# Kernel tuning notes

Hardware: AMD Instinct MI355X
Metric: run time of the kernel (lower is better)

Reference implementation:

```python
import jax, jax.numpy as jnp
import numpy as np

N_OPS = 32
D_REASON = 128
TOP_K = 2
EPS = 1e-05
LEAK = 1e-05  # coefficient on the all-ops leak term


def setup_inputs() -> dict:
    key = jax.random.key(0)
    k1, k2, k3, k4 = jax.random.split(key, 4)
    B, S = 8, 2048
    x = jax.random.normal(k1, (B, S, D_REASON), dtype=jnp.float32)
    indices = jax.random.randint(k2, (B, S, TOP_K), 0, N_OPS, dtype=jnp.int64)
    weights = jax.random.uniform(k3, (B, S, TOP_K), dtype=jnp.float32)
    ops = 0.02 * jax.random.normal(k4, (N_OPS, D_REASON, D_REASON), dtype=jnp.float32)
    return {"x": x, "indices": indices, "weights": weights, "ops": ops}


def _ternary_effective(ops):
    # scale_n = clamp(mean|W_n|, 1e-5); q = STE ternary quantize; W_eff = q * scale
    scale = jnp.maximum(jnp.mean(jnp.abs(ops), axis=(1, 2)), EPS)  # (N,)
    q_hard = jnp.clip(jnp.round(ops / scale[:, None, None]), -1.0, 1.0)
    # STE: identity gradient w.r.t. ops through the quantizer
    q = ops + jax.lax.stop_gradient(q_hard - ops)
    return q * scale[:, None, None]  # (N, D, D)


def reference(x, indices, weights, ops):
    # x: (B,S,D); indices: (B,S,K) int; weights: (B,S,K); ops: (N,D,D)
    w_eff = _ternary_effective(ops)  # (N, D_out, D_in)
    # F.linear(x, W) = x @ W.T, for every op at once -> T: (B,S,N,D_out)
    T = jnp.einsum("bsd,nod->bsno", x, w_eff)
    total = T.sum(axis=2)  # sum over all ops, (B,S,D)
    # gather the selected top_k ops per token: (B,S,K,D)
    gathered = jnp.take_along_axis(T, indices[..., None].astype(jnp.int32), axis=2)
    routed = jnp.sum(weights[..., None] * gathered, axis=2)  # (B,S,D)
    return LEAK * total / N_OPS + routed
```

## Files before the change

### kernel.cpp

```cpp
#include <hip/hip_runtime.h>

#define N_OPS 32
#define D 128
#define MAT (D * D)
#define EPS 1e-5f
#define LEAK 1e-5f
#define NTOK (8 * 2048)
#define NASSIGN (NTOK * 2)
#define CAP 34816
#define EXP_GRPS (CAP / 64)
#define LEAK_BLKS 64

typedef __attribute__((ext_vector_type(8))) short short8;
typedef __attribute__((ext_vector_type(4))) float f32x4;

__device__ inline unsigned short f2bf(float f) {
    unsigned int u = __float_as_uint(f);
    return (unsigned short)((u + 0x7FFF + ((u >> 16) & 1)) >> 16);
}
__device__ inline float bf2f(unsigned short h) {
    return __uint_as_float(((unsigned int)h) << 16);
}

__global__ __launch_bounds__(256) void k_prep(const float* __restrict__ ops,
                                              const int* __restrict__ idx,
                                              const float* __restrict__ x,
                                              float* __restrict__ scale,
                                              int* __restrict__ hist2,
                                              unsigned short* __restrict__ xb) {
    if (blockIdx.x < N_OPS) {
        const int n = blockIdx.x;
        const float* W = ops + n * MAT;
        float s = 0.f;
        for (int i = threadIdx.x; i < MAT; i += 256) s += fabsf(W[i]);
        for (int off = 32; off; off >>= 1) s += __shfl_xor(s, off);
        __shared__ float red[4];
        const int lane = threadIdx.x & 63, wid = threadIdx.x >> 6;
        if (lane == 0) red[wid] = s;
        __syncthreads();
        if (threadIdx.x == 0)
            scale[n] = fmaxf((red[0] + red[1] + red[2] + red[3]) / (float)MAT, EPS);
    } else if (blockIdx.x < 64) {
        const int b = blockIdx.x - N_OPS;
        __shared__ int lh[N_OPS];
        if (threadIdx.x < N_OPS) lh[threadIdx.x] = 0;
        __syncthreads();
#pragma unroll
        for (int j = 0; j < 4; ++j)
            atomicAdd(&lh[idx[b * 1024 + j * 256 + threadIdx.x]], 1);
        __syncthreads();
        if (threadIdx.x < N_OPS) hist2[b * N_OPS + threadIdx.x] = lh[threadIdx.x];
    } else {
        const int gid = (blockIdx.x - 64) * 256 + threadIdx.x;
        const float4* xp = (const float4*)(x + (size_t)gid * 8);
        float4 a = xp[0], b = xp[1];
        unsigned short o[8] = {f2bf(a.x), f2bf(a.y), f2bf(a.z), f2bf(a.w),
                               f2bf(b.x), f2bf(b.y), f2bf(b.z), f2bf(b.w)};
        ((short8*)xb)[gid] = *(const short8*)o;
    }
}

__global__ __launch_bounds__(256) void k_scan_quant(const float* __restrict__ ops,
                                                    const float* __restrict__ scale,
                                                    const int* __restrict__ hist2,
                                                    int* __restrict__ base2,
                                                    int* __restrict__ list,
                                                    unsigned short* __restrict__ wb) {
    if (blockIdx.x == 0) {
        __shared__ int hl[1024];
        __shared__ int totl[N_OPS];
        __shared__ int offl[N_OPS + 1];
        for (int i = threadIdx.x; i < 1024; i += 256) hl[i] = hist2[i];
        __syncthreads();
        if (threadIdx.x < N_OPS) {
            int t = 0;
            for (int b = 0; b < 32; ++b) t += hl[b * N_OPS + threadIdx.x];
            totl[threadIdx.x] = t;
        }
        __syncthreads();
        if (threadIdx.x == 0) {
            int run = 0;
            for (int e = 0; e < N_OPS; ++e) { offl[e] = run; run += (totl[e] + 63) & ~63; }
            offl[N_OPS] = run;
        }
        __syncthreads();
        if (threadIdx.x < N_OPS) {
            const int e = threadIdx.x;
            int running = offl[e];
            for (int b = 0; b < 32; ++b) { base2[b * N_OPS + e] = running; running += hl[b * N_OPS + e]; }
            for (int s = running; s < offl[e + 1]; ++s) list[s] = -1;
        }
        for (int s = offl[N_OPS] + (int)threadIdx.x; s < CAP; s += 256) list[s] = -1;
    } else {
        const int e = blockIdx.x - 1;
        const float sc = scale[e];
        const float* W = ops + e * MAT;
#pragma unroll
        for (int it = 0; it < 8; ++it) {
            const int f = it * 256 + threadIdx.x;
            const int o = f >> 4, dc = f & 15;
            const float4* wp = (const float4*)(W + o * D + dc * 8);
            float4 a = wp[0], b = wp[1];
            float v[8] = {a.x, a.y, a.z, a.w, b.x, b.y, b.z, b.w};
            unsigned short q[8];
#pragma unroll
            for (int j = 0; j < 8; ++j) {
                float t = rintf(v[j] / sc);
                t = fminf(1.f, fmaxf(-1.f, t));
                q[j] = (t == 0.f) ? 0 : (t > 0.f ? 0x3F80 : 0xBF80);
            }
            ((short8*)wb)[e * 2048 + dc * 128 + o] = *(const short8*)q;
        }
    }
}

__global__ __launch_bounds__(256) void k_scatter_leakmat(const int* __restrict__ idx,
                                                         const float* __restrict__ scale,
                                                         const int* __restrict__ base2,
                                                         int* __restrict__ list,
                                                         int* __restrict__ slot_of,
                                                         unsigned short* __restrict__ wb) {
    if (blockIdx.x < 32) {
        const int b = blockIdx.x;
        __shared__ int lh[N_OPS];
        if (threadIdx.x < N_OPS) lh[threadIdx.x] = 0;
        __syncthreads();
#pragma unroll
        for (int j = 0; j < 4; ++j) {
            const int a = b * 1024 + j * 256 + threadIdx.x;
            const int e = idx[a];
            const int r = atomicAdd(&lh[e], 1);
            const int slot = base2[b * N_OPS + e] + r;
            list[slot] = (e << 20) | a;
            slot_of[a] = slot;
        }
    } else {
        const int lb = blockIdx.x - 32;
        const int g  = lb * 32 + (threadIdx.x >> 3);
        const int ec = threadIdx.x & 7;
        float acc[8] = {0, 0, 0, 0, 0, 0, 0, 0};
#pragma unroll
        for (int ee = 0; ee < 4; ++ee) {
            const int e = ec * 4 + ee;
            const float se = scale[e];
            short8 v = ((const short8*)wb)[e * 2048 + g];
#pragma unroll
            for (int j = 0; j < 8; ++j) acc[j] += se * bf2f((unsigned short)v[j]);
        }
#pragma unroll
        for (int m = 1; m <= 4; m <<= 1)
#pragma unroll
            for (int j = 0; j < 8; ++j) acc[j] += __shfl_xor(acc[j], m);
        if (ec == 0) {
            unsigned short o[8];
#pragma unroll
            for (int j = 0; j < 8; ++j) o[j] = f2bf(acc[j] * (LEAK / (float)N_OPS));
            ((short8*)wb)[N_OPS * 2048 + g] = *(const short8*)o;
        }
    }
}

__global__ __launch_bounds__(256, 2) void k_mfma(const unsigned short* __restrict__ xb,
                                                 const int* __restrict__ list,
                                                 const unsigned short* __restrict__ wb,
                                                 const float* __restrict__ scale,
                                                 float* __restrict__ partial,
                                                 float* __restrict__ out) {
    __shared__ short8 lB[2048];
    const int lane = threadIdx.x & 63;
    const int wv   = threadIdx.x >> 6;
    const int quad = lane >> 4;
    const int ncol = lane & 15;

    const bool isleak = blockIdx.x >= EXP_GRPS;
    const short8* src;
    if (isleak) {
        src = (const short8*)wb + N_OPS * 2048;
    } else {
        const int v0 = list[blockIdx.x * 64];
        if (v0 < 0) return;
        src = (const short8*)wb + (v0 >> 20) * 2048;
    }
    for (int i = threadIdx.x; i < 2048; i += 256) lB[i] = src[i];
    __syncthreads();

    const int npass = isleak ? 4 : 1;
    for (int g = 0; g < npass; ++g) {
        int rowbase, tok;
        float sc;
        float* dst;
        if (isleak) {
            rowbase = (blockIdx.x - EXP_GRPS) * 256 + g * 64 + wv * 16;
            tok = rowbase + ncol;
            sc = 1.f;
            dst = out;
        } else {
            rowbase = blockIdx.x * 64 + wv * 16;
            const int v = list[rowbase + ncol];
            tok = (v < 0) ? 0 : ((v & 0xFFFFF) >> 1);
            sc = scale[__builtin_amdgcn_readfirstlane(list[blockIdx.x * 64]) >> 20];
            dst = partial;
        }
        const short8* Ap = (const short8*)(xb + (size_t)tok * D);

        f32x4 acc[8];
#pragma unroll
        for (int j = 0; j < 8; ++j) acc[j] = (f32x4){0.f, 0.f, 0.f, 0.f};

#pragma unroll
        for (int s = 0; s < 4; ++s) {
            const short8 a = Ap[s * 4 + quad];
            const short8* Bp = lB + (s * 4 + quad) * 128;
#pragma unroll
            for (int nt = 0; nt < 8; ++nt) {
                const short8 b = Bp[nt * 16 + ncol];
                acc[nt] = __builtin_amdgcn_mfma_f32_16x16x32_bf16(a, b, acc[nt], 0, 0, 0);
            }
        }
#pragma unroll
        for (int nt = 0; nt < 8; ++nt)
#pragma unroll
            for (int r = 0; r < 4; ++r)
                dst[(size_t)(rowbase + quad * 4 + r) * D + nt * 16 + ncol] = acc[nt][r] * sc;
    }
}

__global__ __launch_bounds__(256) void k_final(const float* __restrict__ partial,
                                               const int* __restrict__ slot_of,
                                               const float* __restrict__ wts,
                                               float* __restrict__ out) {
    const int lane = threadIdx.x & 63;
    const int t = blockIdx.x * 4 + (threadIdx.x >> 6);
    const int s0 = slot_of[2 * t], s1 = slot_of[2 * t + 1];
    const float w0 = wts[2 * t], w1 = wts[2 * t + 1];
    const float2 p0 = ((const float2*)(partial + (size_t)s0 * D))[lane];
    const float2 p1 = ((const float2*)(partial + (size_t)s1 * D))[lane];
    float2* op = ((float2*)out) + (size_t)t * 64 + lane;
    float2 o = *op;
    o.x += w0 * p0.x + w1 * p1.x;
    o.y += w0 * p0.y + w1 * p1.y;
    *op = o;
}

extern "C" void kernel_launch(void* const* d_in, const int* in_sizes, int n_in,
                              void* d_out, int out_size, void* d_ws, size_t ws_size,
                              hipStream_t stream) {
    const float* x   = (const float*)d_in[0];
    const int*   idx = (const int*)  d_in[1];
    const float* wts = (const float*)d_in[2];
    const float* ops = (const float*)d_in[3];
    float* out = (float*)d_out;

    float*          partial = (float*)d_ws;
    unsigned short* xb      = (unsigned short*)(partial + (size_t)CAP * D);
    unsigned short* wb      = xb + (size_t)NTOK * D;
    float*          scale   = (float*)(wb + 33 * MAT);
    int*            hist2   = (int*)(scale + 32);
    int*            base2   = hist2 + 1024;
    int*            list    = base2 + 1024;
    int*            slot_of = list + CAP;

    k_prep<<<1088, 256, 0, stream>>>(ops, idx, x, scale, hist2, xb);
    k_scan_quant<<<33, 256, 0, stream>>>(ops, scale, hist2, base2, list, wb);
    k_scatter_leakmat<<<96, 256, 0, stream>>>(idx, scale, base2, list, slot_of, wb);
    k_mfma<<<EXP_GRPS + LEAK_BLKS, 256, 0, stream>>>(xb, list, wb, scale, partial, out);
    k_final<<<NTOK / 4, 256, 0, stream>>>(partial, slot_of, wts, out);
}
```

Before: 110.3 us.

## Store expert and leak partials in bf16, fuse quantization into prep, enlarge expert blocks

Ternary quantization of the ops now runs inside the scale-reduction blocks of the prep kernel, and the leak matrix is built in the scan kernel. Expert groups are padded to 256 rows, so each MFMA block covers four 64-row passes with one shared B-tile load. Expert partials and leak results are written as bf16 to a separate buffer, and the final kernel combines them without a read-modify-write of out. This is meant to cut global memory traffic and stage count, at the cost of extra bf16 rounding on the partials and more padding rows.

```diff
diff --git a/kernel.cpp b/kernel.cpp
--- a/kernel.cpp
+++ b/kernel.cpp
@@ -7,8 +7,8 @@
 #define LEAK 1e-5f
 #define NTOK (8 * 2048)
 #define NASSIGN (NTOK * 2)
-#define CAP 34816
-#define EXP_GRPS (CAP / 64)
+#define CAP 40960
+#define EXP_BLKS (CAP / 256)
 #define LEAK_BLKS 64
 
 typedef __attribute__((ext_vector_type(8))) short short8;
@@ -27,19 +27,41 @@
                                               const float* __restrict__ x,
                                               float* __restrict__ scale,
                                               int* __restrict__ hist2,
-                                              unsigned short* __restrict__ xb) {
+                                              unsigned short* __restrict__ xb,
+                                              unsigned short* __restrict__ wb) {
     if (blockIdx.x < N_OPS) {
-        const int n = blockIdx.x;
-        const float* W = ops + n * MAT;
+        const int e = blockIdx.x;
+        const float* W = ops + e * MAT;
         float s = 0.f;
         for (int i = threadIdx.x; i < MAT; i += 256) s += fabsf(W[i]);
         for (int off = 32; off; off >>= 1) s += __shfl_xor(s, off);
         __shared__ float red[4];
+        __shared__ float s_scale;
         const int lane = threadIdx.x & 63, wid = threadIdx.x >> 6;
         if (lane == 0) red[wid] = s;
         __syncthreads();
-        if (threadIdx.x == 0)
-            scale[n] = fmaxf((red[0] + red[1] + red[2] + red[3]) / (float)MAT, EPS);
+        if (threadIdx.x == 0) {
+            s_scale = fmaxf((red[0] + red[1] + red[2] + red[3]) / (float)MAT, EPS);
+            scale[e] = s_scale;
+        }
+        __syncthreads();
+        const float sc = s_scale;
+#pragma unroll
+        for (int it = 0; it < 8; ++it) {
+            const int f = it * 256 + threadIdx.x;
+            const int o = f >> 4, dc = f & 15;
+            const float4* wp = (const float4*)(W + o * D + dc * 8);
+            float4 a = wp[0], b = wp[1];
+            float v[8] = {a.x, a.y, a.z, a.w, b.x, b.y, b.z, b.w};
+            unsigned short q[8];
+#pragma unroll
+            for (int j = 0; j < 8; ++j) {
+                float t = rintf(v[j] / sc);
+                t = fminf(1.f, fmaxf(-1.f, t));
+                q[j] = (t == 0.f) ? 0 : (t > 0.f ? 0x3F80 : 0xBF80);
+            }
+            ((short8*)wb)[e * 2048 + dc * 128 + o] = *(const short8*)q;
+        }
     } else if (blockIdx.x < 64) {
         const int b = blockIdx.x - N_OPS;
         __shared__ int lh[N_OPS];
@@ -60,12 +82,11 @@
     }
 }
 
-__global__ __launch_bounds__(256) void k_scan_quant(const float* __restrict__ ops,
-                                                    const float* __restrict__ scale,
-                                                    const int* __restrict__ hist2,
-                                                    int* __restrict__ base2,
-                                                    int* __restrict__ list,
-                                                    unsigned short* __restrict__ wb) {
+__global__ __launch_bounds__(256) void k_scan_leak(const int* __restrict__ hist2,
+                                                   const float* __restrict__ scale,
+                                                   int* __restrict__ base2,
+                                                   int* __restrict__ list,
+                                                   unsigned short* __restrict__ wb) {
     if (blockIdx.x == 0) {
         __shared__ int hl[1024];
         __shared__ int totl[N_OPS];
@@ -80,7 +101,7 @@
         __syncthreads();
         if (threadIdx.x == 0) {
             int run = 0;
-            for (int e = 0; e < N_OPS; ++e) { offl[e] = run; run += (totl[e] + 63) & ~63; }
+            for (int e = 0; e < N_OPS; ++e) { offl[e] = run; run += (totl[e] + 255) & ~255; }
             offl[N_OPS] = run;
         }
         __syncthreads();
@@ -90,52 +111,10 @@
             for (int b = 0; b < 32; ++b) { base2[b * N_OPS + e] = running; running += hl[b * N_OPS + e]; }
             for (int s = running; s < offl[e + 1]; ++s) list[s] = -1;
         }
+        __syncthreads();
         for (int s = offl[N_OPS] + (int)threadIdx.x; s < CAP; s += 256) list[s] = -1;
     } else {
-        const int e = blockIdx.x - 1;
-        const float sc = scale[e];
-        const float* W = ops + e * MAT;
-#pragma unroll
-        for (int it = 0; it < 8; ++it) {
-            const int f = it * 256 + threadIdx.x;
-            const int o = f >> 4, dc = f & 15;
-            const float4* wp = (const float4*)(W + o * D + dc * 8);
-            float4 a = wp[0], b = wp[1];
-            float v[8] = {a.x, a.y, a.z, a.w, b.x, b.y, b.z, b.w};
-            unsigned short q[8];
-#pragma unroll
-            for (int j = 0; j < 8; ++j) {
-                float t = rintf(v[j] / sc);
-                t = fminf(1.f, fmaxf(-1.f, t));
-                q[j] = (t == 0.f) ? 0 : (t > 0.f ? 0x3F80 : 0xBF80);
-            }
-            ((short8*)wb)[e * 2048 + dc * 128 + o] = *(const short8*)q;
-        }
-    }
-}
-
-__global__ __launch_bounds__(256) void k_scatter_leakmat(const int* __restrict__ idx,
-                                                         const float* __restrict__ scale,
-                                                         const int* __restrict__ base2,
-                                                         int* __restrict__ list,
-                                                         int* __restrict__ slot_of,
-                                                         unsigned short* __restrict__ wb) {
-    if (blockIdx.x < 32) {
-        const int b = blockIdx.x;
-        __shared__ int lh[N_OPS];
-        if (threadIdx.x < N_OPS) lh[threadIdx.x] = 0;
-        __syncthreads();
-#pragma unroll
-        for (int j = 0; j < 4; ++j) {
-            const int a = b * 1024 + j * 256 + threadIdx.x;
-            const int e = idx[a];
-            const int r = atomicAdd(&lh[e], 1);
-            const int slot = base2[b * N_OPS + e] + r;
-            list[slot] = (e << 20) | a;
-            slot_of[a] = slot;
-        }
-    } else {
-        const int lb = blockIdx.x - 32;
+        const int lb = blockIdx.x - 1;
         const int g  = lb * 32 + (threadIdx.x >> 3);
         const int ec = threadIdx.x & 7;
         float acc[8] = {0, 0, 0, 0, 0, 0, 0, 0};
@@ -160,46 +139,66 @@
     }
 }
 
+__global__ __launch_bounds__(256) void k_scatter(const int* __restrict__ idx,
+                                                 const int* __restrict__ base2,
+                                                 int* __restrict__ list,
+                                                 int* __restrict__ slot_of) {
+    const int b = blockIdx.x;
+    __shared__ int lh[N_OPS];
+    if (threadIdx.x < N_OPS) lh[threadIdx.x] = 0;
+    __syncthreads();
+#pragma unroll
+    for (int j = 0; j < 4; ++j) {
+        const int a = b * 1024 + j * 256 + threadIdx.x;
+        const int e = idx[a];
+        const int r = atomicAdd(&lh[e], 1);
+        const int slot = base2[b * N_OPS + e] + r;
+        list[slot] = (e << 20) | a;
+        slot_of[a] = slot;
+    }
+}
+
 __global__ __launch_bounds__(256, 2) void k_mfma(const unsigned short* __restrict__ xb,
                                                  const int* __restrict__ list,
                                                  const unsigned short* __restrict__ wb,
                                                  const float* __restrict__ scale,
-                                                 float* __restrict__ partial,
-                                                 float* __restrict__ out) {
+                                                 unsigned short* __restrict__ partial,
+                                                 unsigned short* __restrict__ lp) {
     __shared__ short8 lB[2048];
     const int lane = threadIdx.x & 63;
     const int wv   = threadIdx.x >> 6;
     const int quad = lane >> 4;
     const int ncol = lane & 15;
 
-    const bool isleak = blockIdx.x >= EXP_GRPS;
+    const bool isleak = blockIdx.x >= EXP_BLKS;
+    int base;
     const short8* src;
+    float sc;
+    unsigned short* dst;
     if (isleak) {
+        base = (blockIdx.x - EXP_BLKS) * 256;
         src = (const short8*)wb + N_OPS * 2048;
+        sc = 1.f;
+        dst = lp;
     } else {
-        const int v0 = list[blockIdx.x * 64];
+        base = blockIdx.x * 256;
+        const int v0 = list[base];
         if (v0 < 0) return;
         src = (const short8*)wb + (v0 >> 20) * 2048;
+        sc = scale[v0 >> 20];
+        dst = partial;
     }
     for (int i = threadIdx.x; i < 2048; i += 256) lB[i] = src[i];
     __syncthreads();
 
-    const int npass = isleak ? 4 : 1;
-    for (int g = 0; g < npass; ++g) {
-        int rowbase, tok;
-        float sc;
-        float* dst;
+    for (int g = 0; g < 4; ++g) {
+        const int rowbase = base + g * 64 + wv * 16;
+        int tok;
         if (isleak) {
-            rowbase = (blockIdx.x - EXP_GRPS) * 256 + g * 64 + wv * 16;
             tok = rowbase + ncol;
-            sc = 1.f;
-            dst = out;
         } else {
-            rowbase = blockIdx.x * 64 + wv * 16;
             const int v = list[rowbase + ncol];
             tok = (v < 0) ? 0 : ((v & 0xFFFFF) >> 1);
-            sc = scale[__builtin_amdgcn_readfirstlane(list[blockIdx.x * 64]) >> 20];
-            dst = partial;
         }
         const short8* Ap = (const short8*)(xb + (size_t)tok * D);
 
@@ -221,11 +220,13 @@
         for (int nt = 0; nt < 8; ++nt)
 #pragma unroll
             for (int r = 0; r < 4; ++r)
-                dst[(size_t)(rowbase + quad * 4 + r) * D + nt * 16 + ncol] = acc[nt][r] * sc;
-    }
-}
-
-__global__ __launch_bounds__(256) void k_final(const float* __restrict__ partial,
+                dst[(size_t)(rowbase + quad * 4 + r) * D + nt * 16 + ncol] =
+                    f2bf(acc[nt][r] * sc);
+    }
+}
+
+__global__ __launch_bounds__(256) void k_final(const unsigned short* __restrict__ partial,
+                                               const unsigned short* __restrict__ lp,
                                                const int* __restrict__ slot_of,
                                                const float* __restrict__ wts,
                                                float* __restrict__ out) {
@@ -233,13 +234,17 @@
     const int t = blockIdx.x * 4 + (threadIdx.x >> 6);
     const int s0 = slot_of[2 * t], s1 = slot_of[2 * t + 1];
     const float w0 = wts[2 * t], w1 = wts[2 * t + 1];
-    const float2 p0 = ((const float2*)(partial + (size_t)s0 * D))[lane];
-    const float2 p1 = ((const float2*)(partial + (size_t)s1 * D))[lane];
-    float2* op = ((float2*)out) + (size_t)t * 64 + lane;
-    float2 o = *op;
-    o.x += w0 * p0.x + w1 * p1.x;
-    o.y += w0 * p0.y + w1 * p1.y;
-    *op = o;
+    const unsigned int a0 = ((const unsigned int*)(partial + (size_t)s0 * D))[lane];
+    const unsigned int a1 = ((const unsigned int*)(partial + (size_t)s1 * D))[lane];
+    const unsigned int l  = ((const unsigned int*)(lp + (size_t)t * D))[lane];
+    float2 o;
+    o.x = bf2f((unsigned short)(l & 0xFFFF))
+        + w0 * bf2f((unsigned short)(a0 & 0xFFFF))
+        + w1 * bf2f((unsigned short)(a1 & 0xFFFF));
+    o.y = bf2f((unsigned short)(l >> 16))
+        + w0 * bf2f((unsigned short)(a0 >> 16))
+        + w1 * bf2f((unsigned short)(a1 >> 16));
+    ((float2*)out)[(size_t)t * 64 + lane] = o;
 }
 
 extern "C" void kernel_launch(void* const* d_in, const int* in_sizes, int n_in,
@@ -251,8 +256,9 @@
     const float* ops = (const float*)d_in[3];
     float* out = (float*)d_out;
 
-    float*          partial = (float*)d_ws;
-    unsigned short* xb      = (unsigned short*)(partial + (size_t)CAP * D);
+    unsigned short* partial = (unsigned short*)d_ws;
+    unsigned short* lp      = partial + (size_t)CAP * D;
+    unsigned short* xb      = lp + (size_t)NTOK * D;
     unsigned short* wb      = xb + (size_t)NTOK * D;
     float*          scale   = (float*)(wb + 33 * MAT);
     int*            hist2   = (int*)(scale + 32);
@@ -260,9 +266,9 @@
     int*            list    = base2 + 1024;
     int*            slot_of = list + CAP;
 
-    k_prep<<<1088, 256, 0, stream>>>(ops, idx, x, scale, hist2, xb);
-    k_scan_quant<<<33, 256, 0, stream>>>(ops, scale, hist2, base2, list, wb);
-    k_scatter_leakmat<<<96, 256, 0, stream>>>(idx, scale, base2, list, slot_of, wb);
-    k_mfma<<<EXP_GRPS + LEAK_BLKS, 256, 0, stream>>>(xb, list, wb, scale, partial, out);
-    k_final<<<NTOK / 4, 256, 0, stream>>>(partial, slot_of, wts, out);
-}
+    k_prep<<<1088, 256, 0, stream>>>(ops, idx, x, scale, hist2, xb, wb);
+    k_scan_leak<<<65, 256, 0, stream>>>(hist2, scale, base2, list, wb);
+    k_scatter<<<32, 256, 0, stream>>>(idx, base2, list, slot_of);
+    k_mfma<<<EXP_BLKS + LEAK_BLKS, 256, 0, stream>>>(xb, list, wb, scale, partial, lp);
+    k_final<<<NTOK / 4, 256, 0, stream>>>(partial, lp, slot_of, wts, out);
+}
```

After: 112.0 us. Within noise of the previous version (+1.6%).
